# Performance work log

Measured on AMD Instinct MI355X. Metric: run time of the kernel, lower is better.

## Reference

```python
import jax, jax.numpy as jnp
import numpy as np

B, LQ, LK, D, H, DK = 128, 32, 128, 1024, 16, 64


def setup_inputs() -> dict:
    key = jax.random.key(0)
    ks = jax.random.split(key, 10)
    Q_seq = jax.random.normal(ks[0], (B, LQ, D), dtype=jnp.float32)
    K_seq = jax.random.normal(ks[1], (B, LK, D), dtype=jnp.float32)
    V_seq = jax.random.normal(ks[2], (B, LK, D), dtype=jnp.float32)
    title_mask = (jax.random.uniform(ks[3], (B, LQ)) < 0.9).astype(jnp.float32)
    body_mask = (jax.random.uniform(ks[4], (B, LQ, LK)) < 0.9).astype(jnp.float32)
    s = 1.0 / np.sqrt(D)
    Wq = jax.random.uniform(ks[5], (H * DK, D), jnp.float32, -s, s)
    Wk = jax.random.uniform(ks[6], (H * DK, D), jnp.float32, -s, s)
    Wv = jax.random.uniform(ks[7], (H * DK, D), jnp.float32, -s, s)
    bq = jnp.zeros((H * DK,), jnp.float32)
    bk = jnp.zeros((H * DK,), jnp.float32)
    bv = jnp.zeros((H * DK,), jnp.float32)
    return {"Q_seq": Q_seq, "K_seq": K_seq, "V_seq": V_seq,
            "title_mask": title_mask, "body_mask": body_mask,
            "Wq": Wq, "bq": bq, "Wk": Wk, "bk": bk, "Wv": Wv, "bv": bv}


def reference(Q_seq, K_seq, V_seq, title_mask, body_mask, Wq, bq, Wk, bk, Wv, bv):
    b = Q_seq.shape[0]
    # concatenate title tokens onto keys/values: [B, LK+LQ, D]
    K_cat = jnp.concatenate([K_seq, Q_seq], axis=1)
    V_cat = jnp.concatenate([V_seq, Q_seq], axis=1)
    # mask: [B, LQ, LK+LQ]
    tmask_rep = jnp.broadcast_to(title_mask[:, None, :], (b, LQ, LQ))
    mask = jnp.concatenate([body_mask, tmask_rep], axis=2) * title_mask[:, :, None]
    # projections -> [B, H, len, DK]
    Qh = (Q_seq @ Wq.T + bq).reshape(b, LQ, H, DK).transpose(0, 2, 1, 3)
    Kh = (K_cat @ Wk.T + bk).reshape(b, LK + LQ, H, DK).transpose(0, 2, 1, 3)
    Vh = (V_cat @ Wv.T + bv).reshape(b, LK + LQ, H, DK).transpose(0, 2, 1, 3)
    # custom exp-based masked attention (non-softmax normalization)
    scores = jnp.einsum('bhqd,bhkd->bhqk', Qh, Kh) / np.sqrt(float(DK))
    scores = jnp.exp(scores) * mask[:, None, :, :]
    attn = scores / (jnp.sum(scores, axis=-1, keepdims=True) + 1e-8)
    ctx = jnp.einsum('bhqk,bhkd->bhqd', attn, Vh)
    return ctx.transpose(0, 2, 1, 3).reshape(b, LQ, H * DK)
```

## Files before the change

kernel.cpp:

```cpp
#include <hip/hip_runtime.h>

typedef _Float16 f16;
typedef _Float16 f16x2 __attribute__((ext_vector_type(2)));
typedef _Float16 f16x4 __attribute__((ext_vector_type(4)));
typedef _Float16 f16x8 __attribute__((ext_vector_type(8)));
typedef float f32x4v __attribute__((ext_vector_type(4)));

#define AS1 __attribute__((address_space(1)))
#define AS3 __attribute__((address_space(3)))

__device__ __forceinline__ void gload_lds16(const f16* g, f16* l) {
  __builtin_amdgcn_global_load_lds((const AS1 unsigned int*)g,
                                   (AS3 unsigned int*)l, 16, 0, 0);
}

__global__ __launch_bounds__(256) void prep_kernel(
    const float* __restrict__ Q_seq, const float* __restrict__ K_seq,
    const float* __restrict__ V_seq,
    const float* __restrict__ Wq, const float* __restrict__ Wk,
    const float* __restrict__ Wv,
    f16* __restrict__ Qb, f16* __restrict__ Kb, f16* __restrict__ Vb,
    f16* __restrict__ Wqb, f16* __restrict__ Wkb, f16* __restrict__ Wvb)
{
  const long long g = (long long)blockIdx.x * 256 + threadIdx.x;
  const float* s;
  f16* d;
  if (g < 524288) {
    s = Q_seq + g * 8; d = Qb + g * 8;
  } else if (g < 2621440) {
    long long e = (g - 524288) * 8; s = K_seq + e; d = Kb + e;
  } else if (g < 4718592) {
    long long e = (g - 2621440) * 8; s = V_seq + e; d = Vb + e;
  } else if (g < 4849664) {
    long long e = (g - 4718592) * 8; s = Wq + e; d = Wqb + e;
  } else if (g < 4980736) {
    long long e = (g - 4849664) * 8; s = Wk + e; d = Wkb + e;
  } else {
    long long e = (g - 4980736) * 8; s = Wv + e; d = Wvb + e;
  }
  float4 v0 = *(const float4*)s;
  float4 v1 = *(const float4*)(s + 4);
  f16x8 o;
  o[0] = (f16)v0.x; o[1] = (f16)v0.y; o[2] = (f16)v0.z; o[3] = (f16)v0.w;
  o[4] = (f16)v1.x; o[5] = (f16)v1.y; o[6] = (f16)v1.z; o[7] = (f16)v1.w;
  *(f16x8*)d = o;
}

__device__ __forceinline__ void gemm_tile_256(
    const f16* __restrict__ A, const f16* __restrict__ W,
    const float* __restrict__ bias, f16* __restrict__ C,
    int m0, int n0, int rowShift, int outStride, int rowOff,
    f16* sbuf)
{
  const int t = threadIdx.x;
  const int w = t >> 6, lane = t & 63;
  const int wr = w >> 2, wc = w & 3;
  const int fr = lane & 15, g = lane >> 4;
  const int lrow = lane >> 3;
  const int kgr = (lane & 7) ^ lrow;

  const f16* aSrc[4];
  const f16* bSrc[4];
#pragma unroll
  for (int s = 0; s < 4; ++s) {
    aSrc[s] = A + (long long)(m0 + (w * 4 + s) * 8 + lrow) * 1024 + kgr * 8;
    bSrc[s] = W + (long long)(n0 + (w * 4 + s) * 8 + lrow) * 1024 + kgr * 8;
  }

#define STAGE(tile)                                                          \
  {                                                                          \
    f16* ab_ = sbuf + (((tile) & 1) << 15);                                  \
    const int ko_ = (tile) * 64;                                             \
    _Pragma("unroll") for (int s = 0; s < 4; ++s)                            \
        gload_lds16(aSrc[s] + ko_, ab_ + (w * 4 + s) * 512);                 \
    _Pragma("unroll") for (int s = 0; s < 4; ++s)                            \
        gload_lds16(bSrc[s] + ko_, ab_ + 16384 + (w * 4 + s) * 512);         \
  }

  const int gk0 = ((0 + g) ^ (fr & 7)) * 8;
  const int gk1 = ((4 + g) ^ (fr & 7)) * 8;
  const int aoff = (wr * 128 + fr) * 64;
  const int boff = (wc * 64 + fr) * 64;

  f32x4v acc[8][4];
#pragma unroll
  for (int i = 0; i < 8; ++i)
#pragma unroll
    for (int j = 0; j < 4; ++j) acc[i][j] = (f32x4v){0.f, 0.f, 0.f, 0.f};

  STAGE(0);
  __syncthreads();

  for (int tt = 0; tt < 16; ++tt) {
    const f16* ab = sbuf + ((tt & 1) << 15);
    const f16* bb = ab + 16384;

    if (tt < 15) STAGE(tt + 1);
    __builtin_amdgcn_sched_barrier(0);

    f16x8 a0[8], b0[4], a1[8], b1[4];
#pragma unroll
    for (int i = 0; i < 8; ++i)
      a0[i] = *(const f16x8*)(ab + aoff + i * 1024 + gk0);
#pragma unroll
    for (int j = 0; j < 4; ++j)
      b0[j] = *(const f16x8*)(bb + boff + j * 1024 + gk0);
#pragma unroll
    for (int i = 0; i < 8; ++i)
#pragma unroll
      for (int j = 0; j < 4; ++j)
        acc[i][j] = __builtin_amdgcn_mfma_f32_16x16x32_f16(a0[i], b0[j],
                                                           acc[i][j], 0, 0, 0);
#pragma unroll
    for (int i = 0; i < 8; ++i)
      a1[i] = *(const f16x8*)(ab + aoff + i * 1024 + gk1);
#pragma unroll
    for (int j = 0; j < 4; ++j)
      b1[j] = *(const f16x8*)(bb + boff + j * 1024 + gk1);
#pragma unroll
    for (int i = 0; i < 8; ++i)
#pragma unroll
      for (int j = 0; j < 4; ++j)
        acc[i][j] = __builtin_amdgcn_mfma_f32_16x16x32_f16(a1[i], b1[j],
                                                           acc[i][j], 0, 0, 0);

    __syncthreads();
  }
#undef STAGE

  f16* Cs = sbuf;
  float bn[4];
#pragma unroll
  for (int j = 0; j < 4; ++j) bn[j] = bias[n0 + wc * 64 + j * 16 + fr];
#pragma unroll
  for (int i = 0; i < 8; ++i) {
#pragma unroll
    for (int j = 0; j < 4; ++j) {
#pragma unroll
      for (int v = 0; v < 4; ++v) {
        int row = wr * 128 + i * 16 + g * 4 + v;
        int col = wc * 64 + j * 16 + fr;
        Cs[row * 256 + (col ^ (((row >> 2) & 7) << 3))] =
            (f16)(acc[i][j][v] + bn[j]);
      }
    }
  }
  __syncthreads();

  const int rowMask = (1 << rowShift) - 1;
  const int row = t >> 1, half = t & 1;
  const int csw = ((row >> 2) & 7) << 3;
  const int arow = m0 + row;
  const int orow = (arow >> rowShift) * outStride + (arow & rowMask) + rowOff;
  f16* dst = C + (long long)orow * 1024 + n0 + half * 128;
  const f16* srcr = Cs + row * 256;
#pragma unroll
  for (int c = 0; c < 16; ++c)
    *(f16x8*)(dst + c * 8) = *(const f16x8*)(srcr + ((half * 128 + c * 8) ^ csw));
}

__global__ __launch_bounds__(512, 1) void gemm_all(
    const f16* __restrict__ Qb, const f16* __restrict__ Kb,
    const f16* __restrict__ Vb,
    const f16* __restrict__ Wqb, const f16* __restrict__ Wkb,
    const f16* __restrict__ Wvb,
    const float* __restrict__ bq, const float* __restrict__ bk,
    const float* __restrict__ bv,
    f16* __restrict__ Qh, f16* __restrict__ Kh, f16* __restrict__ Vh)
{
  __shared__ __align__(16) f16 sbuf[65536];
  const int bid = blockIdx.x;
  const int v = (bid & 7) * 88 + (bid >> 3);

  const f16* A;
  const f16* W;
  const float* bias;
  f16* C;
  int m0, n0, rowShift, outStride, rowOff;

  if (v < 512) {
    const int z = v >> 8, rem = v & 255;
    A = z ? Vb : Kb;
    W = z ? Wvb : Wkb;
    bias = z ? bv : bk;
    C = z ? Vh : Kh;
    m0 = (rem >> 2) * 256; n0 = (rem & 3) * 256;
    rowShift = 7; outStride = 160; rowOff = 0;
  } else {
    const int u = v - 512;
    const int z = u >> 6, rem = u & 63;
    A = Qb;
    W = (z == 0) ? Wqb : (z == 1) ? Wkb : Wvb;
    bias = (z == 0) ? bq : (z == 1) ? bk : bv;
    C = (z == 0) ? Qh : (z == 1) ? Kh : Vh;
    m0 = (rem >> 2) * 256; n0 = (rem & 3) * 256;
    rowShift = 5;
    outStride = (z == 0) ? 32 : 160;
    rowOff = (z == 0) ? 0 : 128;
  }
  gemm_tile_256(A, W, bias, C, m0, n0, rowShift, outStride, rowOff, sbuf);
}

__global__ __launch_bounds__(256) void attn_kernel(
    const f16* __restrict__ Qh, const f16* __restrict__ Kh,
    const f16* __restrict__ Vh,
    const float* __restrict__ title, const float* __restrict__ body,
    float* __restrict__ out)
{
  __shared__ __align__(16) f16 Qs[32 * 72];
  __shared__ __align__(16) f16 Ks[160 * 72];
  __shared__ __align__(16) f16 Vs[160 * 68];
  __shared__ float rs[4][32];
  __shared__ float invs[32];

  const int bh = blockIdx.x, b = bh >> 4, h = bh & 15;
  const int t = threadIdx.x, w = t >> 6, lane = t & 63;
  const int c = lane & 15, g = lane >> 4;

  const long long qbase = ((long long)(b * 32) << 10) + h * 64;
  const long long kbase = ((long long)(b * 160) << 10) + h * 64;

  {
    int row = t >> 3, ch = t & 7;
    *(f16x8*)(Qs + row * 72 + ch * 8) =
        *(const f16x8*)(Qh + qbase + (long long)row * 1024 + ch * 8);
  }
#pragma unroll
  for (int r = 0; r < 5; ++r) {
    int i = t + r * 256;
    int row = i >> 3, ch = i & 7;
    *(f16x8*)(Ks + row * 72 + ch * 8) =
        *(const f16x8*)(Kh + kbase + (long long)row * 1024 + ch * 8);
    f16x8 vv = *(const f16x8*)(Vh + kbase + (long long)row * 1024 + ch * 8);
    f16x4 vlo = __builtin_shufflevector(vv, vv, 0, 1, 2, 3);
    f16x4 vhi = __builtin_shufflevector(vv, vv, 4, 5, 6, 7);
    *(f16x4*)(Vs + row * 68 + ch * 8) = vlo;
    *(f16x4*)(Vs + row * 68 + ch * 8 + 4) = vhi;
  }
  __syncthreads();

  f16x8 qf[2][2];
#pragma unroll
  for (int qt = 0; qt < 2; ++qt)
#pragma unroll
    for (int s = 0; s < 2; ++s)
      qf[qt][s] = *(const f16x8*)(Qs + (qt * 16 + c) * 72 + s * 32 + g * 8);

  const int cnt = (w < 2) ? 3 : 2;
  const int tile0 = (w < 2) ? w * 3 : 6 + (w - 2) * 2;

  f16x4 pp[3][2];
  float rsum[2] = {0.f, 0.f};

#pragma unroll
  for (int i = 0; i < 3; ++i) {
    if (i < cnt) {
      const int kt = tile0 + i;
      f16x8 kf0 = *(const f16x8*)(Ks + (kt * 16 + c) * 72 + 0 + g * 8);
      f16x8 kf1 = *(const f16x8*)(Ks + (kt * 16 + c) * 72 + 32 + g * 8);
#pragma unroll
      for (int qt = 0; qt < 2; ++qt) {
        f32x4v s4 = (f32x4v){0.f, 0.f, 0.f, 0.f};
        s4 = __builtin_amdgcn_mfma_f32_16x16x32_f16(kf0, qf[qt][0], s4, 0, 0, 0);
        s4 = __builtin_amdgcn_mfma_f32_16x16x32_f16(kf1, qf[qt][1], s4, 0, 0, 0);
        float4 m4;
        if (kt < 8) {
          m4 = *(const float4*)(body +
                ((long long)(b * 32 + qt * 16 + c)) * 128 + kt * 16 + 4 * g);
        } else {
          m4 = *(const float4*)(title + b * 32 + (kt - 8) * 16 + 4 * g);
        }
        float e0 = __expf(s4[0] * 0.125f) * m4.x;
        float e1 = __expf(s4[1] * 0.125f) * m4.y;
        float e2 = __expf(s4[2] * 0.125f) * m4.z;
        float e3 = __expf(s4[3] * 0.125f) * m4.w;
        rsum[qt] += (e0 + e1) + (e2 + e3);
        f16x4 p4;
        p4.x = (f16)e0; p4.y = (f16)e1; p4.z = (f16)e2; p4.w = (f16)e3;
        pp[i][qt] = p4;
      }
    }
  }

#pragma unroll
  for (int qt = 0; qt < 2; ++qt) {
    rsum[qt] += __shfl_xor(rsum[qt], 16);
    rsum[qt] += __shfl_xor(rsum[qt], 32);
  }
  if (lane < 16) {
    rs[w][c] = rsum[0];
    rs[w][16 + c] = rsum[1];
  }
  __syncthreads();

  f16* Ps = Ks;
#pragma unroll
  for (int i = 0; i < 3; ++i) {
    if (i < cnt) {
      const int kt = tile0 + i;
#pragma unroll
      for (int qt = 0; qt < 2; ++qt)
        *(f16x4*)(Ps + (qt * 16 + c) * 168 + kt * 16 + 4 * g) = pp[i][qt];
    }
  }
  if (t < 32) {
    float ssum = rs[0][t] + rs[1][t] + rs[2][t] + rs[3][t];
    invs[t] = title[b * 32 + t] / (ssum + 1e-8f);
  }
  __syncthreads();

  f32x4v o[2] = {(f32x4v){0.f, 0.f, 0.f, 0.f}, (f32x4v){0.f, 0.f, 0.f, 0.f}};
#pragma unroll
  for (int s = 0; s < 5; ++s) {
    f16x8 vf;
#pragma unroll
    for (int j = 0; j < 8; ++j)
      vf[j] = Vs[(32 * s + 8 * g + j) * 68 + 16 * w + c];
#pragma unroll
    for (int qt = 0; qt < 2; ++qt) {
      f16x8 pf = *(const f16x8*)(Ps + (qt * 16 + c) * 168 + s * 32 + g * 8);
      o[qt] = __builtin_amdgcn_mfma_f32_16x16x32_f16(pf, vf, o[qt], 0, 0, 0);
    }
  }

#pragma unroll
  for (int qt = 0; qt < 2; ++qt) {
#pragma unroll
    for (int v = 0; v < 4; ++v) {
      int q = qt * 16 + 4 * g + v;
      out[((long long)(b * 32 + q) << 10) + h * 64 + 16 * w + c] =
          o[qt][v] * invs[q];
    }
  }
}

extern "C" void kernel_launch(void* const* d_in, const int* in_sizes, int n_in,
                              void* d_out, int out_size, void* d_ws, size_t ws_size,
                              hipStream_t stream) {
  const float* Q_seq = (const float*)d_in[0];
  const float* K_seq = (const float*)d_in[1];
  const float* V_seq = (const float*)d_in[2];
  const float* title = (const float*)d_in[3];
  const float* body  = (const float*)d_in[4];
  const float* Wq = (const float*)d_in[5];
  const float* bq = (const float*)d_in[6];
  const float* Wk = (const float*)d_in[7];
  const float* bk = (const float*)d_in[8];
  const float* Wv = (const float*)d_in[9];
  const float* bv = (const float*)d_in[10];
  float* out = (float*)d_out;

  f16* ws = (f16*)d_ws;
  f16* Qb  = ws;
  f16* Kb  = Qb + 4194304;
  f16* Vb  = Kb + 16777216;
  f16* Wqb = Vb + 16777216;
  f16* Wkb = Wqb + 1048576;
  f16* Wvb = Wkb + 1048576;
  f16* Qh  = Wvb + 1048576;
  f16* Kh  = Qh + 4194304;
  f16* Vh  = Kh + 20971520;

  prep_kernel<<<19968, 256, 0, stream>>>(Q_seq, K_seq, V_seq, Wq, Wk, Wv,
                                         Qb, Kb, Vb, Wqb, Wkb, Wvb);
  gemm_all<<<704, 512, 0, stream>>>(Qb, Kb, Vb, Wqb, Wkb, Wvb,
                                    bq, bk, bv, Qh, Kh, Vh);
  attn_kernel<<<2048, 256, 0, stream>>>(Qh, Kh, Vh, title, body, out);
}
```

Baseline: 182.6 us.

## Fuse fp32-to-fp16 conversion into GEMM staging, drop prep kernel

Removes the separate conversion kernel that wrote fp16 copies of the inputs and weights. The projection GEMM now reads fp32 directly into registers, converts to fp16, and writes into swizzled LDS, with the loads issued before the MFMA loop and the LDS write after it. This saves a full read/write pass over about 170MB of activations plus a kernel launch. The cost is that the GEMM reads twice as many bytes per tile and uses register-staged loads instead of direct global-to-LDS loads. Weights are also re-read in fp32 by many blocks.

```diff
diff --git a/kernel.cpp b/kernel.cpp
--- a/kernel.cpp
+++ b/kernel.cpp
@@ -1,53 +1,12 @@
 #include <hip/hip_runtime.h>
 
 typedef _Float16 f16;
-typedef _Float16 f16x2 __attribute__((ext_vector_type(2)));
 typedef _Float16 f16x4 __attribute__((ext_vector_type(4)));
 typedef _Float16 f16x8 __attribute__((ext_vector_type(8)));
 typedef float f32x4v __attribute__((ext_vector_type(4)));
 
-#define AS1 __attribute__((address_space(1)))
-#define AS3 __attribute__((address_space(3)))
-
-__device__ __forceinline__ void gload_lds16(const f16* g, f16* l) {
-  __builtin_amdgcn_global_load_lds((const AS1 unsigned int*)g,
-                                   (AS3 unsigned int*)l, 16, 0, 0);
-}
-
-__global__ __launch_bounds__(256) void prep_kernel(
-    const float* __restrict__ Q_seq, const float* __restrict__ K_seq,
-    const float* __restrict__ V_seq,
-    const float* __restrict__ Wq, const float* __restrict__ Wk,
-    const float* __restrict__ Wv,
-    f16* __restrict__ Qb, f16* __restrict__ Kb, f16* __restrict__ Vb,
-    f16* __restrict__ Wqb, f16* __restrict__ Wkb, f16* __restrict__ Wvb)
-{
-  const long long g = (long long)blockIdx.x * 256 + threadIdx.x;
-  const float* s;
-  f16* d;
-  if (g < 524288) {
-    s = Q_seq + g * 8; d = Qb + g * 8;
-  } else if (g < 2621440) {
-    long long e = (g - 524288) * 8; s = K_seq + e; d = Kb + e;
-  } else if (g < 4718592) {
-    long long e = (g - 2621440) * 8; s = V_seq + e; d = Vb + e;
-  } else if (g < 4849664) {
-    long long e = (g - 4718592) * 8; s = Wq + e; d = Wqb + e;
-  } else if (g < 4980736) {
-    long long e = (g - 4849664) * 8; s = Wk + e; d = Wkb + e;
-  } else {
-    long long e = (g - 4980736) * 8; s = Wv + e; d = Wvb + e;
-  }
-  float4 v0 = *(const float4*)s;
-  float4 v1 = *(const float4*)(s + 4);
-  f16x8 o;
-  o[0] = (f16)v0.x; o[1] = (f16)v0.y; o[2] = (f16)v0.z; o[3] = (f16)v0.w;
-  o[4] = (f16)v1.x; o[5] = (f16)v1.y; o[6] = (f16)v1.z; o[7] = (f16)v1.w;
-  *(f16x8*)d = o;
-}
-
 __device__ __forceinline__ void gemm_tile_256(
-    const f16* __restrict__ A, const f16* __restrict__ W,
+    const float* __restrict__ A, const float* __restrict__ W,
     const float* __restrict__ bias, f16* __restrict__ C,
     int m0, int n0, int rowShift, int outStride, int rowOff,
     f16* sbuf)
@@ -56,25 +15,38 @@
   const int w = t >> 6, lane = t & 63;
   const int wr = w >> 2, wc = w & 3;
   const int fr = lane & 15, g = lane >> 4;
-  const int lrow = lane >> 3;
-  const int kgr = (lane & 7) ^ lrow;
-
-  const f16* aSrc[4];
-  const f16* bSrc[4];
-#pragma unroll
-  for (int s = 0; s < 4; ++s) {
-    aSrc[s] = A + (long long)(m0 + (w * 4 + s) * 8 + lrow) * 1024 + kgr * 8;
-    bSrc[s] = W + (long long)(n0 + (w * 4 + s) * 8 + lrow) * 1024 + kgr * 8;
-  }
-
-#define STAGE(tile)                                                          \
+  const int srow = lane >> 3;
+  const int scol = lane & 7;
+  const int gph = scol ^ srow;
+
+  const bool isB = (w >= 4);
+  const int rb = (w & 3) * 64;
+  const float* src = isB
+      ? (W + (long long)(n0 + rb + srow) * 1024 + scol * 8)
+      : (A + (long long)(m0 + rb + srow) * 1024 + scol * 8);
+  f16* dstBase = sbuf + (isB ? 16384 : 0) + (rb + srow) * 64 + gph * 8;
+
+  float4 v0[8], v1[8];
+
+#define SLOAD(k0_)                                                           \
   {                                                                          \
-    f16* ab_ = sbuf + (((tile) & 1) << 15);                                  \
-    const int ko_ = (tile) * 64;                                             \
-    _Pragma("unroll") for (int s = 0; s < 4; ++s)                            \
-        gload_lds16(aSrc[s] + ko_, ab_ + (w * 4 + s) * 512);                 \
-    _Pragma("unroll") for (int s = 0; s < 4; ++s)                            \
-        gload_lds16(bSrc[s] + ko_, ab_ + 16384 + (w * 4 + s) * 512);         \
+    _Pragma("unroll") for (int s = 0; s < 8; ++s) {                          \
+      const float* p_ = src + (long long)s * 8192 + (k0_);                   \
+      v0[s] = *(const float4*)p_;                                            \
+      v1[s] = *(const float4*)(p_ + 4);                                      \
+    }                                                                        \
+  }
+#define SWRITE(bufsel)                                                       \
+  {                                                                          \
+    f16* db_ = dstBase + ((bufsel) << 15);                                   \
+    _Pragma("unroll") for (int s = 0; s < 8; ++s) {                          \
+      f16x8 hv_;                                                             \
+      hv_[0] = (f16)v0[s].x; hv_[1] = (f16)v0[s].y;                          \
+      hv_[2] = (f16)v0[s].z; hv_[3] = (f16)v0[s].w;                          \
+      hv_[4] = (f16)v1[s].x; hv_[5] = (f16)v1[s].y;                          \
+      hv_[6] = (f16)v1[s].z; hv_[7] = (f16)v1[s].w;                          \
+      *(f16x8*)(db_ + s * 512) = hv_;                                        \
+    }                                                                        \
   }
 
   const int gk0 = ((0 + g) ^ (fr & 7)) * 8;
@@ -88,14 +60,15 @@
 #pragma unroll
     for (int j = 0; j < 4; ++j) acc[i][j] = (f32x4v){0.f, 0.f, 0.f, 0.f};
 
-  STAGE(0);
+  SLOAD(0);
+  SWRITE(0);
   __syncthreads();
 
   for (int tt = 0; tt < 16; ++tt) {
     const f16* ab = sbuf + ((tt & 1) << 15);
     const f16* bb = ab + 16384;
 
-    if (tt < 15) STAGE(tt + 1);
+    if (tt < 15) SLOAD((tt + 1) * 64);
     __builtin_amdgcn_sched_barrier(0);
 
     f16x8 a0[8], b0[4], a1[8], b1[4];
@@ -124,9 +97,12 @@
         acc[i][j] = __builtin_amdgcn_mfma_f32_16x16x32_f16(a1[i], b1[j],
                                                            acc[i][j], 0, 0, 0);
 
+    if (tt < 15) SWRITE((tt + 1) & 1);
+
     __syncthreads();
   }
-#undef STAGE
+#undef SLOAD
+#undef SWRITE
 
   f16* Cs = sbuf;
   float bn[4];
@@ -160,10 +136,10 @@
 }
 
 __global__ __launch_bounds__(512, 1) void gemm_all(
-    const f16* __restrict__ Qb, const f16* __restrict__ Kb,
-    const f16* __restrict__ Vb,
-    const f16* __restrict__ Wqb, const f16* __restrict__ Wkb,
-    const f16* __restrict__ Wvb,
+    const float* __restrict__ Q_seq, const float* __restrict__ K_seq,
+    const float* __restrict__ V_seq,
+    const float* __restrict__ Wq, const float* __restrict__ Wk,
+    const float* __restrict__ Wv,
     const float* __restrict__ bq, const float* __restrict__ bk,
     const float* __restrict__ bv,
     f16* __restrict__ Qh, f16* __restrict__ Kh, f16* __restrict__ Vh)
@@ -172,16 +148,16 @@
   const int bid = blockIdx.x;
   const int v = (bid & 7) * 88 + (bid >> 3);
 
-  const f16* A;
-  const f16* W;
+  const float* A;
+  const float* W;
   const float* bias;
   f16* C;
   int m0, n0, rowShift, outStride, rowOff;
 
   if (v < 512) {
     const int z = v >> 8, rem = v & 255;
-    A = z ? Vb : Kb;
-    W = z ? Wvb : Wkb;
+    A = z ? V_seq : K_seq;
+    W = z ? Wv : Wk;
     bias = z ? bv : bk;
     C = z ? Vh : Kh;
     m0 = (rem >> 2) * 256; n0 = (rem & 3) * 256;
@@ -189,8 +165,8 @@
   } else {
     const int u = v - 512;
     const int z = u >> 6, rem = u & 63;
-    A = Qb;
-    W = (z == 0) ? Wqb : (z == 1) ? Wkb : Wvb;
+    A = Q_seq;
+    W = (z == 0) ? Wq : (z == 1) ? Wk : Wv;
     bias = (z == 0) ? bq : (z == 1) ? bk : bv;
     C = (z == 0) ? Qh : (z == 1) ? Kh : Vh;
     m0 = (rem >> 2) * 256; n0 = (rem & 3) * 256;
@@ -351,19 +327,11 @@
   float* out = (float*)d_out;
 
   f16* ws = (f16*)d_ws;
-  f16* Qb  = ws;
-  f16* Kb  = Qb + 4194304;
-  f16* Vb  = Kb + 16777216;
-  f16* Wqb = Vb + 16777216;
-  f16* Wkb = Wqb + 1048576;
-  f16* Wvb = Wkb + 1048576;
-  f16* Qh  = Wvb + 1048576;
-  f16* Kh  = Qh + 4194304;
-  f16* Vh  = Kh + 20971520;
-
-  prep_kernel<<<19968, 256, 0, stream>>>(Q_seq, K_seq, V_seq, Wq, Wk, Wv,
-                                         Qb, Kb, Vb, Wqb, Wkb, Wvb);
-  gemm_all<<<704, 512, 0, stream>>>(Qb, Kb, Vb, Wqb, Wkb, Wvb,
+  f16* Qh = ws;
+  f16* Kh = Qh + 4194304;
+  f16* Vh = Kh + 20971520;
+
+  gemm_all<<<704, 512, 0, stream>>>(Q_seq, K_seq, V_seq, Wq, Wk, Wv,
                                     bq, bk, bv, Qh, Kh, Vh);
   attn_kernel<<<2048, 256, 0, stream>>>(Qh, Kh, Vh, title, body, out);
 }
```

Result: slower. 204.4 us (+11.9%).

## Shrink projection GEMM tiles to 128x128 and make prep kernel grid-stride

Applied to the files above, without the earlier changes.

The projection GEMM moves from 256x256 tiles with 512 threads and double-buffered direct-to-LDS loads to 128x128 tiles with 256 threads, a single LDS buffer and about 34KB of shared memory. This gives four times as many blocks and should allow several blocks per CU. In exchange it drops the software prefetch pipeline, so global loads no longer overlap the MFMAs, and each tile gets less operand reuse. The fp32-to-fp16 prep kernel also switches to a grid-stride loop over a fixed 2048-block grid.

```diff
diff --git a/kernel.cpp b/kernel.cpp
--- a/kernel.cpp
+++ b/kernel.cpp
@@ -1,7 +1,6 @@
 #include <hip/hip_runtime.h>
 
 typedef _Float16 f16;
-typedef _Float16 f16x2 __attribute__((ext_vector_type(2)));
 typedef _Float16 f16x4 __attribute__((ext_vector_type(4)));
 typedef _Float16 f16x8 __attribute__((ext_vector_type(8)));
 typedef float f32x4v __attribute__((ext_vector_type(4)));
@@ -22,31 +21,33 @@
     f16* __restrict__ Qb, f16* __restrict__ Kb, f16* __restrict__ Vb,
     f16* __restrict__ Wqb, f16* __restrict__ Wkb, f16* __restrict__ Wvb)
 {
-  const long long g = (long long)blockIdx.x * 256 + threadIdx.x;
-  const float* s;
-  f16* d;
-  if (g < 524288) {
-    s = Q_seq + g * 8; d = Qb + g * 8;
-  } else if (g < 2621440) {
-    long long e = (g - 524288) * 8; s = K_seq + e; d = Kb + e;
-  } else if (g < 4718592) {
-    long long e = (g - 2621440) * 8; s = V_seq + e; d = Vb + e;
-  } else if (g < 4849664) {
-    long long e = (g - 4718592) * 8; s = Wq + e; d = Wqb + e;
-  } else if (g < 4980736) {
-    long long e = (g - 4849664) * 8; s = Wk + e; d = Wkb + e;
-  } else {
-    long long e = (g - 4980736) * 8; s = Wv + e; d = Wvb + e;
-  }
-  float4 v0 = *(const float4*)s;
-  float4 v1 = *(const float4*)(s + 4);
-  f16x8 o;
-  o[0] = (f16)v0.x; o[1] = (f16)v0.y; o[2] = (f16)v0.z; o[3] = (f16)v0.w;
-  o[4] = (f16)v1.x; o[5] = (f16)v1.y; o[6] = (f16)v1.z; o[7] = (f16)v1.w;
-  *(f16x8*)d = o;
-}
-
-__device__ __forceinline__ void gemm_tile_256(
+  for (long long g = (long long)blockIdx.x * 256 + threadIdx.x;
+       g < 5111808; g += (long long)2048 * 256) {
+    const float* s;
+    f16* d;
+    if (g < 524288) {
+      s = Q_seq + g * 8; d = Qb + g * 8;
+    } else if (g < 2621440) {
+      long long e = (g - 524288) * 8; s = K_seq + e; d = Kb + e;
+    } else if (g < 4718592) {
+      long long e = (g - 2621440) * 8; s = V_seq + e; d = Vb + e;
+    } else if (g < 4849664) {
+      long long e = (g - 4718592) * 8; s = Wq + e; d = Wqb + e;
+    } else if (g < 4980736) {
+      long long e = (g - 4849664) * 8; s = Wk + e; d = Wkb + e;
+    } else {
+      long long e = (g - 4980736) * 8; s = Wv + e; d = Wvb + e;
+    }
+    float4 v0 = *(const float4*)s;
+    float4 v1 = *(const float4*)(s + 4);
+    f16x8 o;
+    o[0] = (f16)v0.x; o[1] = (f16)v0.y; o[2] = (f16)v0.z; o[3] = (f16)v0.w;
+    o[4] = (f16)v1.x; o[5] = (f16)v1.y; o[6] = (f16)v1.z; o[7] = (f16)v1.w;
+    *(f16x8*)d = o;
+  }
+}
+
+__device__ __forceinline__ void gemm_tile_128(
     const f16* __restrict__ A, const f16* __restrict__ W,
     const float* __restrict__ bias, f16* __restrict__ C,
     int m0, int n0, int rowShift, int outStride, int rowOff,
@@ -54,94 +55,78 @@
 {
   const int t = threadIdx.x;
   const int w = t >> 6, lane = t & 63;
-  const int wr = w >> 2, wc = w & 3;
+  const int wr = w >> 1, wc = w & 1;
   const int fr = lane & 15, g = lane >> 4;
-  const int lrow = lane >> 3;
-  const int kgr = (lane & 7) ^ lrow;
-
-  const f16* aSrc[4];
-  const f16* bSrc[4];
-#pragma unroll
-  for (int s = 0; s < 4; ++s) {
-    aSrc[s] = A + (long long)(m0 + (w * 4 + s) * 8 + lrow) * 1024 + kgr * 8;
-    bSrc[s] = W + (long long)(n0 + (w * 4 + s) * 8 + lrow) * 1024 + kgr * 8;
-  }
-
-#define STAGE(tile)                                                          \
-  {                                                                          \
-    f16* ab_ = sbuf + (((tile) & 1) << 15);                                  \
-    const int ko_ = (tile) * 64;                                             \
-    _Pragma("unroll") for (int s = 0; s < 4; ++s)                            \
-        gload_lds16(aSrc[s] + ko_, ab_ + (w * 4 + s) * 512);                 \
-    _Pragma("unroll") for (int s = 0; s < 4; ++s)                            \
-        gload_lds16(bSrc[s] + ko_, ab_ + 16384 + (w * 4 + s) * 512);         \
-  }
+  const int kgr = (t & 7) ^ ((t >> 3) & 7);
+
+  const f16* aS = A + (long long)(m0 + (t >> 3)) * 1024 + kgr * 8;
+  const f16* bS = W + (long long)(n0 + (t >> 3)) * 1024 + kgr * 8;
+  f16* lA = sbuf + w * 512;
+  f16* lB = sbuf + 8192 + w * 512;
 
   const int gk0 = ((0 + g) ^ (fr & 7)) * 8;
   const int gk1 = ((4 + g) ^ (fr & 7)) * 8;
-  const int aoff = (wr * 128 + fr) * 64;
+  const int aoff = (wr * 64 + fr) * 64;
   const int boff = (wc * 64 + fr) * 64;
 
-  f32x4v acc[8][4];
-#pragma unroll
-  for (int i = 0; i < 8; ++i)
+  f32x4v acc[4][4];
+#pragma unroll
+  for (int i = 0; i < 4; ++i)
 #pragma unroll
     for (int j = 0; j < 4; ++j) acc[i][j] = (f32x4v){0.f, 0.f, 0.f, 0.f};
 
-  STAGE(0);
-  __syncthreads();
-
   for (int tt = 0; tt < 16; ++tt) {
-    const f16* ab = sbuf + ((tt & 1) << 15);
-    const f16* bb = ab + 16384;
-
-    if (tt < 15) STAGE(tt + 1);
-    __builtin_amdgcn_sched_barrier(0);
-
-    f16x8 a0[8], b0[4], a1[8], b1[4];
-#pragma unroll
-    for (int i = 0; i < 8; ++i)
-      a0[i] = *(const f16x8*)(ab + aoff + i * 1024 + gk0);
+    const int ko = tt * 64;
+#pragma unroll
+    for (int s = 0; s < 4; ++s)
+      gload_lds16(aS + s * 32768 + ko, lA + s * 2048);
+#pragma unroll
+    for (int s = 0; s < 4; ++s)
+      gload_lds16(bS + s * 32768 + ko, lB + s * 2048);
+    __syncthreads();
+
+    f16x8 af[4], bf[4];
+#pragma unroll
+    for (int i = 0; i < 4; ++i)
+      af[i] = *(const f16x8*)(sbuf + aoff + i * 1024 + gk0);
 #pragma unroll
     for (int j = 0; j < 4; ++j)
-      b0[j] = *(const f16x8*)(bb + boff + j * 1024 + gk0);
-#pragma unroll
-    for (int i = 0; i < 8; ++i)
+      bf[j] = *(const f16x8*)(sbuf + 8192 + boff + j * 1024 + gk0);
+#pragma unroll
+    for (int i = 0; i < 4; ++i)
 #pragma unroll
       for (int j = 0; j < 4; ++j)
-        acc[i][j] = __builtin_amdgcn_mfma_f32_16x16x32_f16(a0[i], b0[j],
+        acc[i][j] = __builtin_amdgcn_mfma_f32_16x16x32_f16(af[i], bf[j],
                                                            acc[i][j], 0, 0, 0);
 #pragma unroll
-    for (int i = 0; i < 8; ++i)
-      a1[i] = *(const f16x8*)(ab + aoff + i * 1024 + gk1);
+    for (int i = 0; i < 4; ++i)
+      af[i] = *(const f16x8*)(sbuf + aoff + i * 1024 + gk1);
 #pragma unroll
     for (int j = 0; j < 4; ++j)
-      b1[j] = *(const f16x8*)(bb + boff + j * 1024 + gk1);
-#pragma unroll
-    for (int i = 0; i < 8; ++i)
+      bf[j] = *(const f16x8*)(sbuf + 8192 + boff + j * 1024 + gk1);
+#pragma unroll
+    for (int i = 0; i < 4; ++i)
 #pragma unroll
       for (int j = 0; j < 4; ++j)
-        acc[i][j] = __builtin_amdgcn_mfma_f32_16x16x32_f16(a1[i], b1[j],
+        acc[i][j] = __builtin_amdgcn_mfma_f32_16x16x32_f16(af[i], bf[j],
                                                            acc[i][j], 0, 0, 0);
 
     __syncthreads();
   }
-#undef STAGE
 
   f16* Cs = sbuf;
   float bn[4];
 #pragma unroll
   for (int j = 0; j < 4; ++j) bn[j] = bias[n0 + wc * 64 + j * 16 + fr];
 #pragma unroll
-  for (int i = 0; i < 8; ++i) {
+  for (int i = 0; i < 4; ++i) {
 #pragma unroll
     for (int j = 0; j < 4; ++j) {
 #pragma unroll
       for (int v = 0; v < 4; ++v) {
-        int row = wr * 128 + i * 16 + g * 4 + v;
+        int row = wr * 64 + i * 16 + g * 4 + v;
         int col = wc * 64 + j * 16 + fr;
-        Cs[row * 256 + (col ^ (((row >> 2) & 7) << 3))] =
-            (f16)(acc[i][j][v] + bn[j]);
+        Cs[row * 136 + (col ^ ((row & 12) << 2))] = (f16)(acc[i][j][v] + bn[j]);
       }
     }
   }
@@ -149,17 +134,17 @@
 
   const int rowMask = (1 << rowShift) - 1;
   const int row = t >> 1, half = t & 1;
-  const int csw = ((row >> 2) & 7) << 3;
+  const int rsw = (row & 12) << 2;
   const int arow = m0 + row;
   const int orow = (arow >> rowShift) * outStride + (arow & rowMask) + rowOff;
-  f16* dst = C + (long long)orow * 1024 + n0 + half * 128;
-  const f16* srcr = Cs + row * 256;
-#pragma unroll
-  for (int c = 0; c < 16; ++c)
-    *(f16x8*)(dst + c * 8) = *(const f16x8*)(srcr + ((half * 128 + c * 8) ^ csw));
-}
-
-__global__ __launch_bounds__(512, 1) void gemm_all(
+  f16* dst = C + (long long)orow * 1024 + n0 + half * 64;
+  const f16* srcr = Cs + row * 136;
+#pragma unroll
+  for (int c = 0; c < 8; ++c)
+    *(f16x8*)(dst + c * 8) = *(const f16x8*)(srcr + ((half * 64 + c * 8) ^ rsw));
+}
+
+__global__ __launch_bounds__(256) void gemm_all(
     const f16* __restrict__ Qb, const f16* __restrict__ Kb,
     const f16* __restrict__ Vb,
     const f16* __restrict__ Wqb, const f16* __restrict__ Wkb,
@@ -168,9 +153,9 @@
     const float* __restrict__ bv,
     f16* __restrict__ Qh, f16* __restrict__ Kh, f16* __restrict__ Vh)
 {
-  __shared__ __align__(16) f16 sbuf[65536];
+  __shared__ __align__(16) f16 sbuf[17408];
   const int bid = blockIdx.x;
-  const int v = (bid & 7) * 88 + (bid >> 3);
+  const int v = (bid & 7) * 352 + (bid >> 3);
 
   const f16* A;
   const f16* W;
@@ -178,27 +163,27 @@
   f16* C;
   int m0, n0, rowShift, outStride, rowOff;
 
-  if (v < 512) {
-    const int z = v >> 8, rem = v & 255;
+  if (v < 2048) {
+    const int z = v >> 10, rem = v & 1023;
     A = z ? Vb : Kb;
     W = z ? Wvb : Wkb;
     bias = z ? bv : bk;
     C = z ? Vh : Kh;
-    m0 = (rem >> 2) * 256; n0 = (rem & 3) * 256;
+    m0 = (rem >> 3) * 128; n0 = (rem & 7) * 128;
     rowShift = 7; outStride = 160; rowOff = 0;
   } else {
-    const int u = v - 512;
-    const int z = u >> 6, rem = u & 63;
+    const int u = v - 2048;
+    const int z = u >> 8, rem = u & 255;
     A = Qb;
     W = (z == 0) ? Wqb : (z == 1) ? Wkb : Wvb;
     bias = (z == 0) ? bq : (z == 1) ? bk : bv;
     C = (z == 0) ? Qh : (z == 1) ? Kh : Vh;
-    m0 = (rem >> 2) * 256; n0 = (rem & 3) * 256;
+    m0 = (rem >> 3) * 128; n0 = (rem & 7) * 128;
     rowShift = 5;
     outStride = (z == 0) ? 32 : 160;
     rowOff = (z == 0) ? 0 : 128;
   }
-  gemm_tile_256(A, W, bias, C, m0, n0, rowShift, outStride, rowOff, sbuf);
+  gemm_tile_128(A, W, bias, C, m0, n0, rowShift, outStride, rowOff, sbuf);
 }
 
 __global__ __launch_bounds__(256) void attn_kernel(
@@ -361,9 +346,9 @@
   f16* Kh  = Qh + 4194304;
   f16* Vh  = Kh + 20971520;
 
-  prep_kernel<<<19968, 256, 0, stream>>>(Q_seq, K_seq, V_seq, Wq, Wk, Wv,
-                                         Qb, Kb, Vb, Wqb, Wkb, Wvb);
-  gemm_all<<<704, 512, 0, stream>>>(Qb, Kb, Vb, Wqb, Wkb, Wvb,
-                                    bq, bk, bv, Qh, Kh, Vh);
+  prep_kernel<<<2048, 256, 0, stream>>>(Q_seq, K_seq, V_seq, Wq, Wk, Wv,
+                                        Qb, Kb, Vb, Wqb, Wkb, Wvb);
+  gemm_all<<<2816, 256, 0, stream>>>(Qb, Kb, Vb, Wqb, Wkb, Wvb,
+                                     bq, bk, bv, Qh, Kh, Vh);
   attn_kernel<<<2048, 256, 0, stream>>>(Qh, Kh, Vh, title, body, out);
 }
```

New measurement: 192.3 us. +5.3%, slower.
